# Performance work log

Hardware: AMD Instinct MI355X
Metric: run time of the kernel (lower is better)

## Reference

```python
import jax, jax.numpy as jnp
import numpy as np

BETA = 0.25  # commitment loss weight


def setup_inputs() -> dict:
    key = jax.random.key(0)
    k1, k2 = jax.random.split(key)
    z = jax.random.normal(k1, (16, 256, 64, 64), dtype=jnp.float32)      # encoder latent, NCHW
    codebook = jax.random.normal(k2, (1024, 256), dtype=jnp.float32)     # [n_e, e_dim]
    return {"z": z, "codebook": codebook}


def reference(z, codebook):
    B, C, H, W = z.shape
    z_bhwc = jnp.transpose(z, (0, 2, 3, 1))            # [B,H,W,C]
    zf = z_bhwc.reshape(-1, C)                          # [N,C], N = B*H*W
    # squared L2 distance to every codeword: ||z||^2 + ||e||^2 - 2 z.e
    d = ((zf * zf).sum(axis=1, keepdims=True)
         + (codebook * codebook).sum(axis=1)[None, :]
         - 2.0 * zf @ codebook.T)                       # [N, n_e]
    idx = jnp.argmin(d, axis=1)                         # [N] nearest codeword
    zq = codebook[idx].reshape(B, H, W, C)              # irregular gather
    # VQ loss: codebook term + beta * commitment term
    loss = (BETA * jnp.mean((jax.lax.stop_gradient(zq) - z_bhwc) ** 2)
            + jnp.mean((zq - jax.lax.stop_gradient(z_bhwc)) ** 2))
    # straight-through estimator
    zq_st = z_bhwc + jax.lax.stop_gradient(zq - z_bhwc)
    return jnp.transpose(zq_st, (0, 3, 1, 2)), loss
```

## Files before the change

### kernel.cpp

```cpp
#include <hip/hip_runtime.h>
#include <cfloat>

#define C_DIM 256
#define HW    4096
#define NE    1024
#define NPIX  65536
#define TAU   0.15f
#define ZSTR  264

typedef __attribute__((ext_vector_type(8))) _Float16 half8_t;
typedef __attribute__((ext_vector_type(4))) float floatx4;

__device__ __forceinline__ unsigned int fenc(float f) {
  unsigned int u = __float_as_uint(f);
  return (u & 0x80000000u) ? ~u : (u | 0x80000000u);
}


__global__ __launch_bounds__(256)
void e2_kernel(const float* __restrict__ cb, float* __restrict__ e2) {
  const int wave = (blockIdx.x * 256 + (int)threadIdx.x) >> 6;
  const int lane = threadIdx.x & 63;
  const float4 v = *(const float4*)(cb + (size_t)wave * C_DIM + lane * 4);
  float s = v.x * v.x + v.y * v.y + v.z * v.z + v.w * v.w;
  #pragma unroll
  for (int off = 32; off; off >>= 1) s += __shfl_down(s, off, 64);
  if (lane == 0) e2[wave] = s;
}

__global__ __launch_bounds__(256)
void pack_kernel(const float* __restrict__ cb, _Float16* __restrict__ EhfP) {
  const int g = blockIdx.x >> 3, it = blockIdx.x & 7;
  const int sidx = it * 256 + (int)threadIdx.x;
  const int ks = sidx >> 8, i = (sidx >> 6) & 3, lane = sidx & 63;
  const int ln = lane & 15, quad = lane >> 4;
  const float* src = cb + (size_t)(g * 64 + i * 16 + ln) * C_DIM + ks * 32 + quad * 8;
  const float4 v0 = *(const float4*)(src);
  const float4 v1 = *(const float4*)(src + 4);
  half8_t h;
  h[0] = (_Float16)v0.x; h[1] = (_Float16)v0.y; h[2] = (_Float16)v0.z; h[3] = (_Float16)v0.w;
  h[4] = (_Float16)v1.x; h[5] = (_Float16)v1.y; h[6] = (_Float16)v1.z; h[7] = (_Float16)v1.w;
  *(half8_t*)(EhfP + (size_t)g * 16384 + (size_t)sidx * 8) = h;
}

__global__ __launch_bounds__(256, 2)
void screen_kernel(const float* __restrict__ z, const _Float16* __restrict__ EhfP,
                   const float* __restrict__ e2, int* __restrict__ idx_out,
                   int* __restrict__ clist, int* __restrict__ ccount) {
  __shared__ __align__(16) _Float16 Zl[128 * ZSTR];
  __shared__ float e2l[NE];

  const int tid = threadIdx.x;
  const int ptile = blockIdx.x * 128;
  const int b = ptile >> 12, pb = ptile & 4095;
  const float* zb = z + (size_t)b * (C_DIM * HW) + pb;

  #pragma unroll
  for (int it = 0; it < 16; ++it) {
    const int flat = it * 256 + tid;
    const int p = flat & 127, kb = flat >> 7;
    float f[8];
    #pragma unroll
    for (int j = 0; j < 8; ++j) f[j] = zb[(size_t)(kb * 8 + j) * HW + p];
    half8_t h;
    #pragma unroll
    for (int j = 0; j < 8; ++j) h[j] = (_Float16)f[j];
    *(half8_t*)&Zl[p * ZSTR + kb * 8] = h;
  }
  #pragma unroll
  for (int i = 0; i < 4; ++i) e2l[i * 256 + tid] = e2[i * 256 + tid];
  __syncthreads();

  const int lane = tid & 63;
  const int w = tid >> 6;
  const int wc = w & 1, wp = w >> 1;
  const int ln = lane & 15, quad = lane >> 4;

  const _Float16* aBase = EhfP + (size_t)wc * 16384 + (size_t)lane * 8;
  const char* rowB[4];
  #pragma unroll
  for (int j = 0; j < 4; ++j)
    rowB[j] = (const char*)(&Zl[(wp * 64 + j * 16 + ln) * ZSTR + quad * 8]);

  float d1[4], d2[4]; int i1[4];
  #pragma unroll
  for (int j = 0; j < 4; ++j) { d1[j] = FLT_MAX; d2[j] = FLT_MAX; i1[j] = 0; }

  half8_t abuf[4][4], bbuf[2][4];
  #pragma unroll
  for (int i = 0; i < 4; ++i) abuf[0][i] = *(const half8_t*)(aBase + i * 512);
  #pragma unroll
  for (int i = 0; i < 4; ++i) abuf[1][i] = *(const half8_t*)(aBase + 2048 + i * 512);
  #pragma unroll
  for (int j = 0; j < 4; ++j) bbuf[0][j] = *(const half8_t*)(rowB[j]);

  for (int nc = 0; nc < 8; ++nc) {
    floatx4 acc[4][4];
    #pragma unroll
    for (int i = 0; i < 4; ++i)
      #pragma unroll
      for (int j = 0; j < 4; ++j) acc[i][j] = (floatx4){0.f, 0.f, 0.f, 0.f};

    #pragma unroll
    for (int ks = 0; ks < 8; ++ks) {
      const int s = nc * 8 + ks;
      const int ca = ks & 3;
      const int pa = (ks + 2) & 3;
      const int cbs = ks & 1;
      const int pbs = cbs ^ 1;
      {
        const int sp = s + 2 > 63 ? 63 : s + 2;
        const size_t aoff = (size_t)(sp >> 3) * 32768 + (size_t)(sp & 7) * 2048;
        #pragma unroll
        for (int i = 0; i < 4; ++i) abuf[pa][i] = *(const half8_t*)(aBase + aoff + i * 512);
      }
      {
        const int s1 = s + 1 > 63 ? 63 : s + 1;
        const int bks = s1 & 7;
        #pragma unroll
        for (int j = 0; j < 4; ++j) bbuf[pbs][j] = *(const half8_t*)(rowB[j] + bks * 64);
      }
      #pragma unroll
      for (int i = 0; i < 4; ++i)
        #pragma unroll
        for (int j = 0; j < 4; ++j)
          acc[i][j] = __builtin_amdgcn_mfma_f32_16x16x32_f16(abuf[ca][i], bbuf[cbs][j], acc[i][j], 0, 0, 0);
    }

    const int cwb = nc * 128 + wc * 64;
    #pragma unroll
    for (int i = 0; i < 4; ++i) {
      const int cw0 = cwb + i * 16 + quad * 4;
      float ee[4];
      #pragma unroll
      for (int r = 0; r < 4; ++r) ee[r] = e2l[cw0 + r];
      #pragma unroll
      for (int j = 0; j < 4; ++j) {
        #pragma unroll
        for (int r = 0; r < 4; ++r) {
          const float d = fmaf(-2.0f, acc[i][j][r], ee[r]);
          const bool lt = d < d1[j];
          const float hi = lt ? d1[j] : d;
          d1[j] = lt ? d : d1[j];
          i1[j] = lt ? (cw0 + r) : i1[j];
          d2[j] = fminf(d2[j], hi);
        }
      }
    }
  }

  #pragma unroll
  for (int j = 0; j < 4; ++j) {
    #pragma unroll
    for (int m = 16; m <= 32; m <<= 1) {
      const float od1 = __shfl_xor(d1[j], m, 64);
      const int   oi1 = __shfl_xor(i1[j], m, 64);
      const float od2 = __shfl_xor(d2[j], m, 64);
      const bool take = (od1 < d1[j]) || (od1 == d1[j] && oi1 < i1[j]);
      const float hi = take ? d1[j] : od1;
      d1[j] = take ? od1 : d1[j];
      i1[j] = take ? oi1 : i1[j];
      d2[j] = fminf(fminf(d2[j], od2), hi);
    }
  }

  __syncthreads();
  float* rd1 = (float*)Zl;
  int*   ri1 = (int*)Zl + 256;
  float* rd2 = (float*)Zl + 512;
  if (lane < 16) {
    #pragma unroll
    for (int j = 0; j < 4; ++j) {
      const int p = wp * 64 + j * 16 + ln;
      rd1[wc * 128 + p] = d1[j];
      ri1[wc * 128 + p] = i1[j];
      rd2[wc * 128 + p] = d2[j];
    }
  }
  __syncthreads();
  if (tid < 128) {
    const float a1 = rd1[tid], b1 = rd1[128 + tid];
    const int   ai = ri1[tid], bi = ri1[128 + tid];
    const float a2 = rd2[tid], b2 = rd2[128 + tid];
    const bool take = (b1 < a1) || (b1 == a1 && bi < ai);
    const float d1f = take ? b1 : a1;
    const int   i1f = take ? bi : ai;
    const float hi  = take ? a1 : b1;
    const float d2f = fminf(fminf(a2, b2), hi);
    const int gp = ptile + tid;
    idx_out[gp] = i1f;
    if ((d2f - d1f) <= TAU) {
      const int pos = atomicAdd(ccount, 1);
      clist[pos] = gp;
    }
  }
}

__global__ __launch_bounds__(256)
void rescan_kernel(const float* __restrict__ z, const float* __restrict__ cb,
                   const float* __restrict__ e2, const int* __restrict__ clist,
                   const int* __restrict__ ccount, int* __restrict__ idx_out) {
  __shared__ __align__(16) float zl[4][C_DIM];
  __shared__ int pxs[4];
  __shared__ unsigned long long bestk[4];
  const int n = *ccount;
  const int ngroups = (n + 3) >> 2;
  for (int g = blockIdx.x; g < ngroups; g += gridDim.x) {
    const int base = g * 4;
    if ((int)threadIdx.x < 4) {
      pxs[threadIdx.x] = clist[min(base + (int)threadIdx.x, n - 1)];
      bestk[threadIdx.x] = ~0ULL;
    }
    __syncthreads();
    {
      const int k = threadIdx.x;
      #pragma unroll
      for (int i = 0; i < 4; ++i) {
        const int gp = pxs[i];
        zl[i][k] = z[(size_t)(gp >> 12) * (C_DIM * HW) + (size_t)k * HW + (gp & 4095)];
      }
    }
    __syncthreads();
    unsigned long long mykey[4] = {~0ULL, ~0ULL, ~0ULL, ~0ULL};
    #pragma unroll 1
    for (int o = 0; o < 4; ++o) {
      const int cw = o * 256 + (int)threadIdx.x;
      const float* row = cb + (size_t)cw * C_DIM;
      float dot[4] = {0.f, 0.f, 0.f, 0.f};
      #pragma unroll 4
      for (int k0 = 0; k0 < C_DIM; k0 += 4) {
        const float4 ev = *(const float4*)(row + k0);
        #pragma unroll
        for (int i = 0; i < 4; ++i) {
          const float4 zz = *(const float4*)&zl[i][k0];
          dot[i] = fmaf(ev.x, zz.x, dot[i]);
          dot[i] = fmaf(ev.y, zz.y, dot[i]);
          dot[i] = fmaf(ev.z, zz.z, dot[i]);
          dot[i] = fmaf(ev.w, zz.w, dot[i]);
        }
      }
      const float ee = e2[cw];
      #pragma unroll
      for (int i = 0; i < 4; ++i) {
        const float d = fmaf(-2.0f, dot[i], ee);
        const unsigned long long key = ((unsigned long long)fenc(d) << 32) | (unsigned)cw;
        mykey[i] = key < mykey[i] ? key : mykey[i];
      }
    }
    #pragma unroll
    for (int i = 0; i < 4; ++i) {
      unsigned long long k = mykey[i];
      #pragma unroll
      for (int off = 32; off; off >>= 1) {
        const unsigned long long ok = __shfl_xor(k, off, 64);
        k = ok < k ? ok : k;
      }
      if ((threadIdx.x & 63) == 0) atomicMin(&bestk[i], k);
    }
    __syncthreads();
    if ((int)threadIdx.x < 4)
      idx_out[pxs[threadIdx.x]] = (int)(unsigned)(bestk[threadIdx.x] & 0xFFFFFFFFull);
    __syncthreads();
  }
}

__global__ __launch_bounds__(256)
void gather_loss_kernel(const float* __restrict__ z, const float* __restrict__ cb,
                        const int* __restrict__ idx,
                        float* __restrict__ out, float* __restrict__ acc) {
  const int pg = blockIdx.x * 256 + threadIdx.x;
  const int id = idx[pg];
  const int b = pg >> 12, p = pg & 4095;
  const float* zrow = z   + (size_t)b * (C_DIM * HW) + p;
  float*       orow = out + (size_t)b * (C_DIM * HW) + p;
  const float* erow = cb + (size_t)id * C_DIM;
  float s = 0.f;
  for (int c0 = 0; c0 < C_DIM; c0 += 4) {
    const float4 ev = *(const float4*)(erow + c0);
    const float e[4] = {ev.x, ev.y, ev.z, ev.w};
    #pragma unroll
    for (int j = 0; j < 4; ++j) {
      const float zv = zrow[(size_t)(c0 + j) * HW];
      const float dd = e[j] - zv;
      s = fmaf(dd, dd, s);
      orow[(size_t)(c0 + j) * HW] = e[j];
    }
  }
  __shared__ float sdata[256];
  sdata[threadIdx.x] = s;
  __syncthreads();
  #pragma unroll
  for (int off = 128; off; off >>= 1) {
    if (threadIdx.x < (unsigned)off) sdata[threadIdx.x] += sdata[threadIdx.x + off];
    __syncthreads();
  }
  if (threadIdx.x == 0) atomicAdd(acc, sdata[0]);
}

__global__ void finalize_kernel(const float* __restrict__ acc, float* __restrict__ loss_out) {
  *loss_out = 1.25f * (*acc) * (1.0f / 16777216.0f);
}

extern "C" void kernel_launch(void* const* d_in, const int* in_sizes, int n_in,
                              void* d_out, int out_size, void* d_ws, size_t ws_size,
                              hipStream_t stream) {
  const float* z  = (const float*)d_in[0];
  const float* cb = (const float*)d_in[1];
  float* out = (float*)d_out;
  char* ws = (char*)d_ws;

  float*    acc    = (float*)ws;
  int*      ccount = (int*)(ws + 8);
  float*    e2     = (float*)(ws + 4096);
  _Float16* EhfP   = (_Float16*)(ws + 8192);
  int*      idx    = (int*)(ws + 532480);
  int*      clist  = (int*)(ws + 794624);

  (void)hipMemsetAsync(d_ws, 0, 16, stream);
  e2_kernel<<<NE / 4, 256, 0, stream>>>(cb, e2);
  pack_kernel<<<128, 256, 0, stream>>>(cb, EhfP);
  screen_kernel<<<NPIX / 128, 256, 0, stream>>>(z, EhfP, e2, idx, clist, ccount);
  rescan_kernel<<<1024, 256, 0, stream>>>(z, cb, e2, clist, ccount, idx);
  gather_loss_kernel<<<NPIX / 256, 256, 0, stream>>>(z, cb, idx, out, acc);
  finalize_kernel<<<1, 1, 0, stream>>>(acc, out + 16777216);
}
```

Before: 228.9 us.

## Halve screen tile, raise occupancy, fuse prep kernels, split gather by channels

The screen kernel now handles 64 pixels per block instead of 128. It uses smaller accumulator and prefetch register arrays and shallower A-prefetch double buffering, and launch bounds allow 4 blocks per CU, all aimed at more waves in flight to hide memory latency. The two codebook preprocessing kernels are merged into one launch. The gather/loss kernel splits each pixel's 256 channels across 4 waves, so there are 4x more blocks and more parallelism. In exchange, each codebook tile is reused by fewer pixels per block, so global codebook traffic rises, and prefetch distance is shorter.

```diff
diff --git a/kernel.cpp b/kernel.cpp
--- a/kernel.cpp
+++ b/kernel.cpp
@@ -18,47 +18,48 @@
 
 
 __global__ __launch_bounds__(256)
-void e2_kernel(const float* __restrict__ cb, float* __restrict__ e2) {
-  const int wave = (blockIdx.x * 256 + (int)threadIdx.x) >> 6;
-  const int lane = threadIdx.x & 63;
-  const float4 v = *(const float4*)(cb + (size_t)wave * C_DIM + lane * 4);
-  float s = v.x * v.x + v.y * v.y + v.z * v.z + v.w * v.w;
-  #pragma unroll
-  for (int off = 32; off; off >>= 1) s += __shfl_down(s, off, 64);
-  if (lane == 0) e2[wave] = s;
-}
-
-__global__ __launch_bounds__(256)
-void pack_kernel(const float* __restrict__ cb, _Float16* __restrict__ EhfP) {
-  const int g = blockIdx.x >> 3, it = blockIdx.x & 7;
-  const int sidx = it * 256 + (int)threadIdx.x;
-  const int ks = sidx >> 8, i = (sidx >> 6) & 3, lane = sidx & 63;
-  const int ln = lane & 15, quad = lane >> 4;
-  const float* src = cb + (size_t)(g * 64 + i * 16 + ln) * C_DIM + ks * 32 + quad * 8;
-  const float4 v0 = *(const float4*)(src);
-  const float4 v1 = *(const float4*)(src + 4);
-  half8_t h;
-  h[0] = (_Float16)v0.x; h[1] = (_Float16)v0.y; h[2] = (_Float16)v0.z; h[3] = (_Float16)v0.w;
-  h[4] = (_Float16)v1.x; h[5] = (_Float16)v1.y; h[6] = (_Float16)v1.z; h[7] = (_Float16)v1.w;
-  *(half8_t*)(EhfP + (size_t)g * 16384 + (size_t)sidx * 8) = h;
-}
-
-__global__ __launch_bounds__(256, 2)
+void prep_kernel(const float* __restrict__ cb, _Float16* __restrict__ EhfP,
+                 float* __restrict__ e2) {
+  if (blockIdx.x < 128) {
+    const int g = blockIdx.x >> 3, it = blockIdx.x & 7;
+    const int sidx = it * 256 + (int)threadIdx.x;
+    const int ks = sidx >> 8, i = (sidx >> 6) & 3, lane = sidx & 63;
+    const int ln = lane & 15, quad = lane >> 4;
+    const float* src = cb + (size_t)(g * 64 + i * 16 + ln) * C_DIM + ks * 32 + quad * 8;
+    const float4 v0 = *(const float4*)(src);
+    const float4 v1 = *(const float4*)(src + 4);
+    half8_t h;
+    h[0] = (_Float16)v0.x; h[1] = (_Float16)v0.y; h[2] = (_Float16)v0.z; h[3] = (_Float16)v0.w;
+    h[4] = (_Float16)v1.x; h[5] = (_Float16)v1.y; h[6] = (_Float16)v1.z; h[7] = (_Float16)v1.w;
+    *(half8_t*)(EhfP + (size_t)g * 16384 + (size_t)sidx * 8) = h;
+  } else {
+    const int bid = blockIdx.x - 128;
+    const int wave = (bid * 256 + (int)threadIdx.x) >> 6;
+    const int lane = threadIdx.x & 63;
+    const float4 v = *(const float4*)(cb + (size_t)wave * C_DIM + lane * 4);
+    float s = v.x * v.x + v.y * v.y + v.z * v.z + v.w * v.w;
+    #pragma unroll
+    for (int off = 32; off; off >>= 1) s += __shfl_down(s, off, 64);
+    if (lane == 0) e2[wave] = s;
+  }
+}
+
+__global__ __launch_bounds__(256, 4)
 void screen_kernel(const float* __restrict__ z, const _Float16* __restrict__ EhfP,
                    const float* __restrict__ e2, int* __restrict__ idx_out,
                    int* __restrict__ clist, int* __restrict__ ccount) {
-  __shared__ __align__(16) _Float16 Zl[128 * ZSTR];
+  __shared__ __align__(16) _Float16 Zl[64 * ZSTR];
   __shared__ float e2l[NE];
 
   const int tid = threadIdx.x;
-  const int ptile = blockIdx.x * 128;
+  const int ptile = blockIdx.x * 64;
   const int b = ptile >> 12, pb = ptile & 4095;
   const float* zb = z + (size_t)b * (C_DIM * HW) + pb;
 
   #pragma unroll
-  for (int it = 0; it < 16; ++it) {
+  for (int it = 0; it < 8; ++it) {
     const int flat = it * 256 + tid;
-    const int p = flat & 127, kb = flat >> 7;
+    const int p = flat & 63, kb = flat >> 6;
     float f[8];
     #pragma unroll
     for (int j = 0; j < 8; ++j) f[j] = zb[(size_t)(kb * 8 + j) * HW + p];
@@ -77,54 +78,44 @@
   const int ln = lane & 15, quad = lane >> 4;
 
   const _Float16* aBase = EhfP + (size_t)wc * 16384 + (size_t)lane * 8;
-  const char* rowB[4];
-  #pragma unroll
-  for (int j = 0; j < 4; ++j)
-    rowB[j] = (const char*)(&Zl[(wp * 64 + j * 16 + ln) * ZSTR + quad * 8]);
-
-  float d1[4], d2[4]; int i1[4];
-  #pragma unroll
-  for (int j = 0; j < 4; ++j) { d1[j] = FLT_MAX; d2[j] = FLT_MAX; i1[j] = 0; }
-
-  half8_t abuf[4][4], bbuf[2][4];
+  const char* rowB[2];
+  #pragma unroll
+  for (int j = 0; j < 2; ++j)
+    rowB[j] = (const char*)(&Zl[(wp * 32 + j * 16 + ln) * ZSTR + quad * 8]);
+
+  float d1[2], d2[2]; int i1[2];
+  #pragma unroll
+  for (int j = 0; j < 2; ++j) { d1[j] = FLT_MAX; d2[j] = FLT_MAX; i1[j] = 0; }
+
+  half8_t abuf[2][4], bbuf[2][2];
   #pragma unroll
   for (int i = 0; i < 4; ++i) abuf[0][i] = *(const half8_t*)(aBase + i * 512);
   #pragma unroll
-  for (int i = 0; i < 4; ++i) abuf[1][i] = *(const half8_t*)(aBase + 2048 + i * 512);
-  #pragma unroll
-  for (int j = 0; j < 4; ++j) bbuf[0][j] = *(const half8_t*)(rowB[j]);
+  for (int j = 0; j < 2; ++j) bbuf[0][j] = *(const half8_t*)(rowB[j]);
 
   for (int nc = 0; nc < 8; ++nc) {
-    floatx4 acc[4][4];
+    floatx4 acc[4][2];
     #pragma unroll
     for (int i = 0; i < 4; ++i)
       #pragma unroll
-      for (int j = 0; j < 4; ++j) acc[i][j] = (floatx4){0.f, 0.f, 0.f, 0.f};
+      for (int j = 0; j < 2; ++j) acc[i][j] = (floatx4){0.f, 0.f, 0.f, 0.f};
 
     #pragma unroll
     for (int ks = 0; ks < 8; ++ks) {
       const int s = nc * 8 + ks;
-      const int ca = ks & 3;
-      const int pa = (ks + 2) & 3;
-      const int cbs = ks & 1;
-      const int pbs = cbs ^ 1;
-      {
-        const int sp = s + 2 > 63 ? 63 : s + 2;
-        const size_t aoff = (size_t)(sp >> 3) * 32768 + (size_t)(sp & 7) * 2048;
-        #pragma unroll
-        for (int i = 0; i < 4; ++i) abuf[pa][i] = *(const half8_t*)(aBase + aoff + i * 512);
-      }
-      {
-        const int s1 = s + 1 > 63 ? 63 : s + 1;
-        const int bks = s1 & 7;
-        #pragma unroll
-        for (int j = 0; j < 4; ++j) bbuf[pbs][j] = *(const half8_t*)(rowB[j] + bks * 64);
-      }
+      const int cur = ks & 1, nxt = cur ^ 1;
+      const int sp = s + 1 > 63 ? 63 : s + 1;
+      const size_t aoff = (size_t)(sp >> 3) * 32768 + (size_t)(sp & 7) * 2048;
+      #pragma unroll
+      for (int i = 0; i < 4; ++i) abuf[nxt][i] = *(const half8_t*)(aBase + aoff + i * 512);
+      const int bks = sp & 7;
+      #pragma unroll
+      for (int j = 0; j < 2; ++j) bbuf[nxt][j] = *(const half8_t*)(rowB[j] + bks * 64);
       #pragma unroll
       for (int i = 0; i < 4; ++i)
         #pragma unroll
-        for (int j = 0; j < 4; ++j)
-          acc[i][j] = __builtin_amdgcn_mfma_f32_16x16x32_f16(abuf[ca][i], bbuf[cbs][j], acc[i][j], 0, 0, 0);
+        for (int j = 0; j < 2; ++j)
+          acc[i][j] = __builtin_amdgcn_mfma_f32_16x16x32_f16(abuf[cur][i], bbuf[cur][j], acc[i][j], 0, 0, 0);
     }
 
     const int cwb = nc * 128 + wc * 64;
@@ -135,7 +126,7 @@
       #pragma unroll
       for (int r = 0; r < 4; ++r) ee[r] = e2l[cw0 + r];
       #pragma unroll
-      for (int j = 0; j < 4; ++j) {
+      for (int j = 0; j < 2; ++j) {
         #pragma unroll
         for (int r = 0; r < 4; ++r) {
           const float d = fmaf(-2.0f, acc[i][j][r], ee[r]);
@@ -150,7 +141,7 @@
   }
 
   #pragma unroll
-  for (int j = 0; j < 4; ++j) {
+  for (int j = 0; j < 2; ++j) {
     #pragma unroll
     for (int m = 16; m <= 32; m <<= 1) {
       const float od1 = __shfl_xor(d1[j], m, 64);
@@ -166,22 +157,22 @@
 
   __syncthreads();
   float* rd1 = (float*)Zl;
-  int*   ri1 = (int*)Zl + 256;
-  float* rd2 = (float*)Zl + 512;
+  int*   ri1 = (int*)Zl + 128;
+  float* rd2 = (float*)Zl + 256;
   if (lane < 16) {
     #pragma unroll
-    for (int j = 0; j < 4; ++j) {
-      const int p = wp * 64 + j * 16 + ln;
-      rd1[wc * 128 + p] = d1[j];
-      ri1[wc * 128 + p] = i1[j];
-      rd2[wc * 128 + p] = d2[j];
+    for (int j = 0; j < 2; ++j) {
+      const int p = wp * 32 + j * 16 + ln;
+      rd1[wc * 64 + p] = d1[j];
+      ri1[wc * 64 + p] = i1[j];
+      rd2[wc * 64 + p] = d2[j];
     }
   }
   __syncthreads();
-  if (tid < 128) {
-    const float a1 = rd1[tid], b1 = rd1[128 + tid];
-    const int   ai = ri1[tid], bi = ri1[128 + tid];
-    const float a2 = rd2[tid], b2 = rd2[128 + tid];
+  if (tid < 64) {
+    const float a1 = rd1[tid], b1 = rd1[64 + tid];
+    const int   ai = ri1[tid], bi = ri1[64 + tid];
+    const float a2 = rd2[tid], b2 = rd2[64 + tid];
     const bool take = (b1 < a1) || (b1 == a1 && bi < ai);
     const float d1f = take ? b1 : a1;
     const int   i1f = take ? bi : ai;
@@ -268,14 +259,16 @@
 void gather_loss_kernel(const float* __restrict__ z, const float* __restrict__ cb,
                         const int* __restrict__ idx,
                         float* __restrict__ out, float* __restrict__ acc) {
-  const int pg = blockIdx.x * 256 + threadIdx.x;
-  const int id = idx[pg];
-  const int b = pg >> 12, p = pg & 4095;
+  const int tid = threadIdx.x;
+  const int px = blockIdx.x * 64 + (tid & 63);
+  const int cbase = (tid >> 6) * 64;
+  const int id = idx[px];
+  const int b = px >> 12, p = px & 4095;
   const float* zrow = z   + (size_t)b * (C_DIM * HW) + p;
   float*       orow = out + (size_t)b * (C_DIM * HW) + p;
   const float* erow = cb + (size_t)id * C_DIM;
   float s = 0.f;
-  for (int c0 = 0; c0 < C_DIM; c0 += 4) {
+  for (int c0 = cbase; c0 < cbase + 64; c0 += 4) {
     const float4 ev = *(const float4*)(erow + c0);
     const float e[4] = {ev.x, ev.y, ev.z, ev.w};
     #pragma unroll
@@ -287,14 +280,14 @@
     }
   }
   __shared__ float sdata[256];
-  sdata[threadIdx.x] = s;
+  sdata[tid] = s;
   __syncthreads();
   #pragma unroll
   for (int off = 128; off; off >>= 1) {
-    if (threadIdx.x < (unsigned)off) sdata[threadIdx.x] += sdata[threadIdx.x + off];
-    __syncthreads();
-  }
-  if (threadIdx.x == 0) atomicAdd(acc, sdata[0]);
+    if (tid < off) sdata[tid] += sdata[tid + off];
+    __syncthreads();
+  }
+  if (tid == 0) atomicAdd(acc, sdata[0]);
 }
 
 __global__ void finalize_kernel(const float* __restrict__ acc, float* __restrict__ loss_out) {
@@ -317,10 +310,9 @@
   int*      clist  = (int*)(ws + 794624);
 
   (void)hipMemsetAsync(d_ws, 0, 16, stream);
-  e2_kernel<<<NE / 4, 256, 0, stream>>>(cb, e2);
-  pack_kernel<<<128, 256, 0, stream>>>(cb, EhfP);
-  screen_kernel<<<NPIX / 128, 256, 0, stream>>>(z, EhfP, e2, idx, clist, ccount);
+  prep_kernel<<<384, 256, 0, stream>>>(cb, EhfP, e2);
+  screen_kernel<<<NPIX / 64, 256, 0, stream>>>(z, EhfP, e2, idx, clist, ccount);
   rescan_kernel<<<1024, 256, 0, stream>>>(z, cb, e2, clist, ccount, idx);
-  gather_loss_kernel<<<NPIX / 256, 256, 0, stream>>>(z, cb, idx, out, acc);
+  gather_loss_kernel<<<NPIX / 64, 256, 0, stream>>>(z, cb, idx, out, acc);
   finalize_kernel<<<1, 1, 0, stream>>>(acc, out + 16777216);
 }
```

Result: slower. 239.0 us (+4.4%).
